# Kernel tuning notes

Hardware: AMD Instinct MI355X
Metric: run time of the kernel (lower is better)

## Reference

```python
import jax, jax.numpy as jnp
import numpy as np

N_PARTS = 24


def setup_inputs() -> dict:
    key = jax.random.key(0)
    k1, k2, k3, k4 = jax.random.split(key, 4)
    B, C, R = 8, 16, 512
    H = W = 512
    tex = jax.random.normal(k1, (B, C, R, R), dtype=jnp.float32)
    # iuv: channel 0 = part id in [0, 24] (0 == background), channels 1,2 = UV bytes in [0, 255]
    part = jax.random.randint(k2, (B, 1, H, W), 0, N_PARTS + 1, dtype=jnp.int32)
    uv = jax.random.randint(k3, (B, 2, H, W), 0, 256, dtype=jnp.int32)
    iuv = jnp.concatenate([part, uv], axis=1)
    lut = jax.random.uniform(k4, (N_PARTS, 256, 256, 2), dtype=jnp.float32)
    return {"tex": tex, "iuv": iuv, "lut": lut, "tex_res": R}


def reference(tex, iuv, lut, tex_res):
    # tex: [B, C, R, R], iuv: [B, 3, H, W] int, lut: [24, 256, 256, 2]
    B = tex.shape[0]
    mask = iuv[:, 0] > 0                                   # [B, H, W]
    i = jnp.clip(iuv[:, 0] - 1, 0, lut.shape[0] - 1)       # part index, clamped for masked-out pixels
    u = jnp.clip(iuv[:, 1].astype(jnp.float32) / 255.0, 0.0, 1.0)
    v = jnp.clip(iuv[:, 2].astype(jnp.float32) / 255.0, 0.0, 1.0)
    ui = jnp.round(u * 255.0).astype(jnp.int32)
    vi = jnp.round(v * 255.0).astype(jnp.int32)
    uv_smpl = lut[i, vi, ui]                               # [B, H, W, 2]
    u_I = jnp.round(uv_smpl[..., 0] * (tex_res - 1)).astype(jnp.int32)
    v_I = jnp.round((1.0 - uv_smpl[..., 1]) * (tex_res - 1)).astype(jnp.int32)
    b_idx = jnp.arange(B)[:, None, None]                   # [B, 1, 1]
    gathered = tex[b_idx, :, v_I, u_I]                     # [B, H, W, C]
    out = jnp.where(mask[..., None], gathered, jnp.zeros((), tex.dtype))
    return jnp.transpose(out, (0, 3, 1, 2))                # [B, C, H, W]
```

## Files before the change

kernel.cpp:

```cpp
#include <hip/hip_runtime.h>


#define N_PARTS 24

__global__ __launch_bounds__(256) void dp_transpose_kernel(
    const float* __restrict__ tex,
    float*       __restrict__ texT)
{
    constexpr int C = 16, R = 512;
    constexpr size_t plane = (size_t)R * R;
    __shared__ float lds[16 * 516];

    const int tid = blockIdx.x;
    const int b  = tid >> 9;
    const int ty = tid & 511;
    const float* src = tex + (size_t)b * C * plane + (size_t)ty * R;
    const int t = threadIdx.x;

    #pragma unroll
    for (int k = 0; k < 8; ++k) {
        const int f  = k * 256 + t;
        const int c  = f >> 7;
        const int x4 = f & 127;
        const float4 v = *(const float4*)(src + (size_t)c * plane + x4 * 4);
        *(float4*)&lds[c * 516 + x4 * 4] = v;
    }
    __syncthreads();
    float* dst = texT + ((size_t)b * plane + (size_t)ty * R) * C;
    #pragma unroll
    for (int k = 0; k < 8; ++k) {
        const int f  = k * 256 + t;
        const int x  = f >> 2;
        const int c0 = (f & 3) * 4;
        float4 v;
        v.x = lds[(c0 + 0) * 516 + x];
        v.y = lds[(c0 + 1) * 516 + x];
        v.z = lds[(c0 + 2) * 516 + x];
        v.w = lds[(c0 + 3) * 516 + x];
        *(float4*)(dst + (size_t)f * 4) = v;
    }
}

__global__ __launch_bounds__(256) void dp_gatherT_kernel(
    const float* __restrict__ texT,
    const int*   __restrict__ iuv,
    const float* __restrict__ lut,
    float*       __restrict__ out)
{
    constexpr int C = 16, R = 512;
    constexpr size_t HW = 512 * 512;
    __shared__ float lds[16 * 256];
    __shared__ int   offs_lds[1024];

    const int b     = blockIdx.x & 7;
    const int inner = blockIdx.x >> 3;
    const int base  = inner * 1024;
    const int t = threadIdx.x;

    {
        const float scale = (float)(R - 1);
        const int pix4 = base + 4 * t;
        const size_t ibase = (size_t)b * 3 * HW + pix4;
        const int4 p4 = *(const int4*)(iuv + ibase);
        const int4 u4 = *(const int4*)(iuv + ibase + HW);
        const int4 v4 = *(const int4*)(iuv + ibase + 2 * HW);

        const int parts[4] = {p4.x, p4.y, p4.z, p4.w};
        const int us[4]    = {u4.x, u4.y, u4.z, u4.w};
        const int vs[4]    = {v4.x, v4.y, v4.z, v4.w};

        int4 o4; int* o = &o4.x;
        #pragma unroll
        for (int j = 0; j < 4; ++j) {
            int i = parts[j] - 1;
            i = i < 0 ? 0 : (i > N_PARTS - 1 ? N_PARTS - 1 : i);
            const float fu = fminf(fmaxf((float)us[j] / 255.0f, 0.0f), 1.0f);
            const float fv = fminf(fmaxf((float)vs[j] / 255.0f, 0.0f), 1.0f);
            const int ui = (int)rintf(fu * 255.0f);
            const int vi = (int)rintf(fv * 255.0f);
            const float2 s = *(const float2*)(lut + (((size_t)i * 256 + vi) * 256 + ui) * 2);
            const int uI = (int)rintf(s.x * scale);
            const int vI = (int)rintf((1.0f - s.y) * scale);
            o[j] = (parts[j] > 0) ? (vI * R + uI) : -1;
        }
        *(int4*)&offs_lds[4 * t] = o4;
    }
    __syncthreads();

    const float* tb   = texT + (size_t)b * HW * C;
    float*       outb = out  + (size_t)b * C * HW + base;

    for (int tile = 0; tile < 4; ++tile) {
        const int p = tile * 256 + t;
        const int o = offs_lds[p];
        const bool m = o >= 0;
        const float4* src = (const float4*)(tb + (size_t)(m ? o : 0) * C);
        float4 r0 = src[0];
        float4 r1 = src[1];
        float4 r2 = src[2];
        float4 r3 = src[3];
        if (!m) {
            r0 = r1 = r2 = r3 = make_float4(0.f, 0.f, 0.f, 0.f);
        }

        if (tile) __syncthreads();
        lds[ 0 * 256 + t] = r0.x;  lds[ 1 * 256 + t] = r0.y;
        lds[ 2 * 256 + t] = r0.z;  lds[ 3 * 256 + t] = r0.w;
        lds[ 4 * 256 + t] = r1.x;  lds[ 5 * 256 + t] = r1.y;
        lds[ 6 * 256 + t] = r1.z;  lds[ 7 * 256 + t] = r1.w;
        lds[ 8 * 256 + t] = r2.x;  lds[ 9 * 256 + t] = r2.y;
        lds[10 * 256 + t] = r2.z;  lds[11 * 256 + t] = r2.w;
        lds[12 * 256 + t] = r3.x;  lds[13 * 256 + t] = r3.y;
        lds[14 * 256 + t] = r3.z;  lds[15 * 256 + t] = r3.w;
        __syncthreads();

        #pragma unroll
        for (int k = 0; k < 4; ++k) {
            const int idx = k * 256 + t;
            const int c   = idx >> 6;
            const int p4  = idx & 63;
            const float4 v = *(const float4*)&lds[c * 256 + p4 * 4];
            *(float4*)(outb + (size_t)c * HW + tile * 256 + p4 * 4) = v;
        }
    }
}

__global__ __launch_bounds__(256) void dp_offsets_kernel(
    const int*   __restrict__ iuv,
    const float* __restrict__ lut,
    int*         __restrict__ offs,
    int R)
{
    constexpr int H = 512, W = 512;
    const float scale = (float)(R - 1);
    const size_t hw = (size_t)H * W;
    const int t = blockIdx.x * blockDim.x + threadIdx.x;
    const int pix4 = t * 4;
    const int b = pix4 >> 18;
    const int p = pix4 & (int)(hw - 1);

    const size_t ibase = (size_t)b * 3 * hw + p;
    const int4 p4 = *(const int4*)(iuv + ibase);
    const int4 u4 = *(const int4*)(iuv + ibase + hw);
    const int4 v4 = *(const int4*)(iuv + ibase + 2 * hw);

    const int parts[4] = {p4.x, p4.y, p4.z, p4.w};
    const int us[4]    = {u4.x, u4.y, u4.z, u4.w};
    const int vs[4]    = {v4.x, v4.y, v4.z, v4.w};

    int4 o4; int* o = &o4.x;
    #pragma unroll
    for (int j = 0; j < 4; ++j) {
        int i = parts[j] - 1;
        i = i < 0 ? 0 : (i > N_PARTS - 1 ? N_PARTS - 1 : i);
        const float fu = fminf(fmaxf((float)us[j] / 255.0f, 0.0f), 1.0f);
        const float fv = fminf(fmaxf((float)vs[j] / 255.0f, 0.0f), 1.0f);
        const int ui = (int)rintf(fu * 255.0f);
        const int vi = (int)rintf(fv * 255.0f);
        const float2 s = *(const float2*)(lut + (((size_t)i * 256 + vi) * 256 + ui) * 2);
        const int uI = (int)rintf(s.x * scale);
        const int vI = (int)rintf((1.0f - s.y) * scale);
        o[j] = (parts[j] > 0) ? (vI * R + uI) : -1;
    }
    *(int4*)(offs + (size_t)b * hw + p) = o4;
}

__global__ __launch_bounds__(256) void dp_gather_kernel(
    const float* __restrict__ tex,
    const int*   __restrict__ offs,
    float*       __restrict__ out,
    int R)
{
    constexpr int C = 16, H = 512, W = 512;
    const size_t hw    = (size_t)H * W;
    const size_t plane = (size_t)R * R;

    const int bid  = blockIdx.x;
    const int xcd  = bid & 7;
    const int slot = bid >> 3;
    const int pl_local = slot >> 8;
    const int inner    = slot & 255;
    const int pidx = xcd * 16 + pl_local;
    const int b = pidx >> 4;
    const int c = pidx & 15;

    const int px = inner * 1024 + threadIdx.x * 4;

    const int4 o4 = *(const int4*)(offs + (size_t)b * hw + px);
    const float* tc = tex + ((size_t)b * C + c) * plane;

    float4 r;
    r.x = (o4.x >= 0) ? tc[o4.x] : 0.0f;
    r.y = (o4.y >= 0) ? tc[o4.y] : 0.0f;
    r.z = (o4.z >= 0) ? tc[o4.z] : 0.0f;
    r.w = (o4.w >= 0) ? tc[o4.w] : 0.0f;

    *(float4*)(out + ((size_t)b * C + c) * hw + px) = r;
}

extern "C" void kernel_launch(void* const* d_in, const int* in_sizes, int n_in,
                              void* d_out, int out_size, void* d_ws, size_t ws_size,
                              hipStream_t stream) {
    const float* tex = (const float*)d_in[0];
    const int*   iuv = (const int*)d_in[1];
    const float* lut = (const float*)d_in[2];
    float*       out = (float*)d_out;

    constexpr int B = 8, C = 16, H = 512, W = 512;
    int R = 512;
    {
        long long pe = (long long)in_sizes[0] / (B * C);
        int r = 1; while ((long long)(r + 1) * (r + 1) <= pe) ++r;
        R = r;
    }

    const size_t texT_bytes = (size_t)B * R * R * C * sizeof(float);
    const size_t offs_bytes = (size_t)B * H * W * sizeof(int);

    if (R == 512 && ws_size >= texT_bytes) {
        float* texT = (float*)d_ws;
        dp_transpose_kernel<<<dim3(4096), dim3(256), 0, stream>>>(tex, texT);
        dp_gatherT_kernel<<<dim3(2048), dim3(256), 0, stream>>>(
            texT, iuv, lut, out);
    } else if (ws_size >= offs_bytes) {
        int* offs = (int*)d_ws;
        dp_offsets_kernel<<<dim3(B * H * W / 4 / 256), dim3(256), 0, stream>>>(
            iuv, lut, offs, R);
        dp_gather_kernel<<<dim3(B * C * (H * W / 1024)), dim3(256), 0, stream>>>(
            tex, offs, out, R);
    }
}
```

Before: 349.7 us.

## Split offset computation into separate kernel, add nontemporal loads/stores, limit gather occupancy

The fused gather kernel used to compute LUT-based texel offsets itself. That work now runs in a separate offsets kernel that writes to workspace, and the gather kernel reads those precomputed offsets. Streaming loads and stores are now marked nontemporal so they do not pollute cache, which is meant to keep cache capacity for the random texT gathers. The gather launch also requests 45056 bytes of dynamic LDS padding to cap occupancy. The trade-offs are an extra kernel launch, an extra round trip of offsets through memory, and a larger workspace requirement.

```diff
diff --git a/kernel.cpp b/kernel.cpp
--- a/kernel.cpp
+++ b/kernel.cpp
@@ -2,6 +2,9 @@
 
 
 #define N_PARTS 24
+
+typedef float v4f __attribute__((ext_vector_type(4)));
+typedef int   v4i __attribute__((ext_vector_type(4)));
 
 __global__ __launch_bounds__(256) void dp_transpose_kernel(
     const float* __restrict__ tex,
@@ -22,8 +25,9 @@
         const int f  = k * 256 + t;
         const int c  = f >> 7;
         const int x4 = f & 127;
-        const float4 v = *(const float4*)(src + (size_t)c * plane + x4 * 4);
-        *(float4*)&lds[c * 516 + x4 * 4] = v;
+        const v4f v = __builtin_nontemporal_load(
+            (const v4f*)(src + (size_t)c * plane + x4 * 4));
+        *(v4f*)&lds[c * 516 + x4 * 4] = v;
     }
     __syncthreads();
     float* dst = texT + ((size_t)b * plane + (size_t)ty * R) * C;
@@ -32,96 +36,12 @@
         const int f  = k * 256 + t;
         const int x  = f >> 2;
         const int c0 = (f & 3) * 4;
-        float4 v;
+        v4f v;
         v.x = lds[(c0 + 0) * 516 + x];
         v.y = lds[(c0 + 1) * 516 + x];
         v.z = lds[(c0 + 2) * 516 + x];
         v.w = lds[(c0 + 3) * 516 + x];
-        *(float4*)(dst + (size_t)f * 4) = v;
-    }
-}
-
-__global__ __launch_bounds__(256) void dp_gatherT_kernel(
-    const float* __restrict__ texT,
-    const int*   __restrict__ iuv,
-    const float* __restrict__ lut,
-    float*       __restrict__ out)
-{
-    constexpr int C = 16, R = 512;
-    constexpr size_t HW = 512 * 512;
-    __shared__ float lds[16 * 256];
-    __shared__ int   offs_lds[1024];
-
-    const int b     = blockIdx.x & 7;
-    const int inner = blockIdx.x >> 3;
-    const int base  = inner * 1024;
-    const int t = threadIdx.x;
-
-    {
-        const float scale = (float)(R - 1);
-        const int pix4 = base + 4 * t;
-        const size_t ibase = (size_t)b * 3 * HW + pix4;
-        const int4 p4 = *(const int4*)(iuv + ibase);
-        const int4 u4 = *(const int4*)(iuv + ibase + HW);
-        const int4 v4 = *(const int4*)(iuv + ibase + 2 * HW);
-
-        const int parts[4] = {p4.x, p4.y, p4.z, p4.w};
-        const int us[4]    = {u4.x, u4.y, u4.z, u4.w};
-        const int vs[4]    = {v4.x, v4.y, v4.z, v4.w};
-
-        int4 o4; int* o = &o4.x;
-        #pragma unroll
-        for (int j = 0; j < 4; ++j) {
-            int i = parts[j] - 1;
-            i = i < 0 ? 0 : (i > N_PARTS - 1 ? N_PARTS - 1 : i);
-            const float fu = fminf(fmaxf((float)us[j] / 255.0f, 0.0f), 1.0f);
-            const float fv = fminf(fmaxf((float)vs[j] / 255.0f, 0.0f), 1.0f);
-            const int ui = (int)rintf(fu * 255.0f);
-            const int vi = (int)rintf(fv * 255.0f);
-            const float2 s = *(const float2*)(lut + (((size_t)i * 256 + vi) * 256 + ui) * 2);
-            const int uI = (int)rintf(s.x * scale);
-            const int vI = (int)rintf((1.0f - s.y) * scale);
-            o[j] = (parts[j] > 0) ? (vI * R + uI) : -1;
-        }
-        *(int4*)&offs_lds[4 * t] = o4;
-    }
-    __syncthreads();
-
-    const float* tb   = texT + (size_t)b * HW * C;
-    float*       outb = out  + (size_t)b * C * HW + base;
-
-    for (int tile = 0; tile < 4; ++tile) {
-        const int p = tile * 256 + t;
-        const int o = offs_lds[p];
-        const bool m = o >= 0;
-        const float4* src = (const float4*)(tb + (size_t)(m ? o : 0) * C);
-        float4 r0 = src[0];
-        float4 r1 = src[1];
-        float4 r2 = src[2];
-        float4 r3 = src[3];
-        if (!m) {
-            r0 = r1 = r2 = r3 = make_float4(0.f, 0.f, 0.f, 0.f);
-        }
-
-        if (tile) __syncthreads();
-        lds[ 0 * 256 + t] = r0.x;  lds[ 1 * 256 + t] = r0.y;
-        lds[ 2 * 256 + t] = r0.z;  lds[ 3 * 256 + t] = r0.w;
-        lds[ 4 * 256 + t] = r1.x;  lds[ 5 * 256 + t] = r1.y;
-        lds[ 6 * 256 + t] = r1.z;  lds[ 7 * 256 + t] = r1.w;
-        lds[ 8 * 256 + t] = r2.x;  lds[ 9 * 256 + t] = r2.y;
-        lds[10 * 256 + t] = r2.z;  lds[11 * 256 + t] = r2.w;
-        lds[12 * 256 + t] = r3.x;  lds[13 * 256 + t] = r3.y;
-        lds[14 * 256 + t] = r3.z;  lds[15 * 256 + t] = r3.w;
-        __syncthreads();
-
-        #pragma unroll
-        for (int k = 0; k < 4; ++k) {
-            const int idx = k * 256 + t;
-            const int c   = idx >> 6;
-            const int p4  = idx & 63;
-            const float4 v = *(const float4*)&lds[c * 256 + p4 * 4];
-            *(float4*)(outb + (size_t)c * HW + tile * 256 + p4 * 4) = v;
-        }
+        __builtin_nontemporal_store(v, (v4f*)(dst + (size_t)f * 4));
     }
 }
 
@@ -140,15 +60,15 @@
     const int p = pix4 & (int)(hw - 1);
 
     const size_t ibase = (size_t)b * 3 * hw + p;
-    const int4 p4 = *(const int4*)(iuv + ibase);
-    const int4 u4 = *(const int4*)(iuv + ibase + hw);
-    const int4 v4 = *(const int4*)(iuv + ibase + 2 * hw);
+    const v4i p4 = __builtin_nontemporal_load((const v4i*)(iuv + ibase));
+    const v4i u4 = __builtin_nontemporal_load((const v4i*)(iuv + ibase + hw));
+    const v4i v4 = __builtin_nontemporal_load((const v4i*)(iuv + ibase + 2 * hw));
 
     const int parts[4] = {p4.x, p4.y, p4.z, p4.w};
     const int us[4]    = {u4.x, u4.y, u4.z, u4.w};
     const int vs[4]    = {v4.x, v4.y, v4.z, v4.w};
 
-    int4 o4; int* o = &o4.x;
+    v4i o4;
     #pragma unroll
     for (int j = 0; j < 4; ++j) {
         int i = parts[j] - 1;
@@ -160,9 +80,66 @@
         const float2 s = *(const float2*)(lut + (((size_t)i * 256 + vi) * 256 + ui) * 2);
         const int uI = (int)rintf(s.x * scale);
         const int vI = (int)rintf((1.0f - s.y) * scale);
-        o[j] = (parts[j] > 0) ? (vI * R + uI) : -1;
-    }
-    *(int4*)(offs + (size_t)b * hw + p) = o4;
+        const int o = (parts[j] > 0) ? (vI * R + uI) : -1;
+        if (j == 0) o4.x = o; else if (j == 1) o4.y = o;
+        else if (j == 2) o4.z = o; else o4.w = o;
+    }
+    __builtin_nontemporal_store(o4, (v4i*)(offs + (size_t)b * hw + p));
+}
+
+__global__ __launch_bounds__(256) void dp_gatherT_kernel(
+    const float* __restrict__ texT,
+    const int*   __restrict__ offs,
+    float*       __restrict__ out)
+{
+    constexpr int C = 16;
+    constexpr size_t HW = 512 * 512;
+    __shared__ float lds[16 * 256];
+    extern __shared__ float occupancy_pad[];
+
+    const int b     = blockIdx.x & 7;
+    const int inner = blockIdx.x >> 3;
+    const int base  = inner * 1024;
+
+    const float* tb   = texT + (size_t)b * HW * C;
+    const int*   ob   = offs + (size_t)b * HW + base;
+    float*       outb = out  + (size_t)b * C * HW + base;
+    const int t = threadIdx.x;
+
+    for (int tile = 0; tile < 4; ++tile) {
+        const int p = tile * 256 + t;
+        const int o = __builtin_nontemporal_load(ob + p);
+        const bool m = o >= 0;
+        const v4f* src = (const v4f*)(tb + (size_t)(m ? o : 0) * C);
+        v4f r0 = src[0];
+        v4f r1 = src[1];
+        v4f r2 = src[2];
+        v4f r3 = src[3];
+        if (!m) {
+            r0 = 0.f; r1 = 0.f; r2 = 0.f; r3 = 0.f;
+        }
+
+        if (tile) __syncthreads();
+        lds[ 0 * 256 + t] = r0.x;  lds[ 1 * 256 + t] = r0.y;
+        lds[ 2 * 256 + t] = r0.z;  lds[ 3 * 256 + t] = r0.w;
+        lds[ 4 * 256 + t] = r1.x;  lds[ 5 * 256 + t] = r1.y;
+        lds[ 6 * 256 + t] = r1.z;  lds[ 7 * 256 + t] = r1.w;
+        lds[ 8 * 256 + t] = r2.x;  lds[ 9 * 256 + t] = r2.y;
+        lds[10 * 256 + t] = r2.z;  lds[11 * 256 + t] = r2.w;
+        lds[12 * 256 + t] = r3.x;  lds[13 * 256 + t] = r3.y;
+        lds[14 * 256 + t] = r3.z;  lds[15 * 256 + t] = r3.w;
+        __syncthreads();
+
+        #pragma unroll
+        for (int k = 0; k < 4; ++k) {
+            const int idx = k * 256 + t;
+            const int c   = idx >> 6;
+            const int p4  = idx & 63;
+            const v4f v = *(const v4f*)&lds[c * 256 + p4 * 4];
+            __builtin_nontemporal_store(
+                v, (v4f*)(outb + (size_t)c * HW + tile * 256 + p4 * 4));
+        }
+    }
 }
 
 __global__ __launch_bounds__(256) void dp_gather_kernel(
@@ -217,11 +194,14 @@
     const size_t texT_bytes = (size_t)B * R * R * C * sizeof(float);
     const size_t offs_bytes = (size_t)B * H * W * sizeof(int);
 
-    if (R == 512 && ws_size >= texT_bytes) {
+    if (R == 512 && ws_size >= texT_bytes + offs_bytes) {
         float* texT = (float*)d_ws;
+        int*   offs = (int*)((char*)d_ws + texT_bytes);
         dp_transpose_kernel<<<dim3(4096), dim3(256), 0, stream>>>(tex, texT);
-        dp_gatherT_kernel<<<dim3(2048), dim3(256), 0, stream>>>(
-            texT, iuv, lut, out);
+        dp_offsets_kernel<<<dim3(B * H * W / 4 / 256), dim3(256), 0, stream>>>(
+            iuv, lut, offs, R);
+        dp_gatherT_kernel<<<dim3(2048), dim3(256), 45056, stream>>>(
+            texT, offs, out);
     } else if (ws_size >= offs_bytes) {
         int* offs = (int*)d_ws;
         dp_offsets_kernel<<<dim3(B * H * W / 4 / 256), dim3(256), 0, stream>>>(
```

Result: no change. 346.2 us (-1.0%).
